# Performance work log

Hardware: AMD Instinct MI355X
Metric: run time of the kernel (lower is better)

The kernel has to match this reference:

```python
import jax, jax.numpy as jnp
import numpy as np

B, L, D = 16, 2048, 128
NEG = -1.0e9


def setup_inputs() -> dict:
    key = jax.random.key(0)
    kq, kk, kv, km = jax.random.split(key, 4)
    Q = jax.random.normal(kq, (B, L, D), dtype=jnp.float32)
    K = jax.random.normal(kk, (B, L, D), dtype=jnp.float32)
    V = jax.random.normal(kv, (B, L, D), dtype=jnp.float32)
    scale = jnp.float32(1.0 / np.sqrt(D))
    # original code masks rows where (mask + 1) == 0, i.e. mask == -1
    mask = jnp.where(jax.random.uniform(km, (B, L)) < 0.1, -1, 0).astype(jnp.int32)
    return {"Q": Q, "K": K, "V": V, "scale": scale, "mask": mask}


def reference(Q, K, V, scale, mask):
    # attention = Q @ K^T * scale  -> [B, Lq, Lk]
    att = jnp.einsum("bqd,bkd->bqk", Q, K) * scale
    # mask[b, i] broadcast over the key dim j (row-wise masking, as in the
    # original unsqueeze(-1).expand pattern with square attention)
    row_masked = (mask + 1) == 0  # [B, L]
    att = jnp.where(row_masked[:, :, None], NEG, att)
    att = jax.nn.softmax(att, axis=-1)
    context = jnp.einsum("bqk,bkd->bqd", att, V)
    return context
```

## Files before the change

kernel.cpp:

```cpp
#include <hip/hip_runtime.h>


#define NB 16
#define LL 2048
#define DD 128
#define LOG2E 1.44269504f
#define NM (-9.0f * 1.44269504f)

typedef __attribute__((ext_vector_type(8))) short short8;
typedef __attribute__((ext_vector_type(16))) float f32x16;

__device__ __forceinline__ float wexp2(float x) {
  float r; asm("v_exp_f32 %0, %1" : "=v"(r) : "v"(x)); return r;
}
__device__ __forceinline__ unsigned cvtpk(float lo, float hi) {
  unsigned r; asm("v_cvt_pk_bf16_f32 %0, %1, %2" : "=v"(r) : "v"(lo), "v"(hi)); return r;
}
__device__ __forceinline__ void gll16(const void* g, const void* l) {
  __builtin_amdgcn_global_load_lds(
      (const __attribute__((address_space(1))) unsigned*)g,
      (__attribute__((address_space(3))) unsigned*)l, 16, 0, 0);
}

__global__ void prep_kv(const float* __restrict__ K, const float* __restrict__ V,
                        short* __restrict__ Kb, short* __restrict__ Vt) {
  __shared__ short lds[64 * 130];
  int bid = blockIdx.x;
  int t = threadIdx.x;
  if (bid < 2048) {
    int g = bid * 256 + t;
    const float4* kp = (const float4*)K + (size_t)g * 2;
    float4 a = kp[0], c = kp[1];
    ((uint4*)Kb)[g] = make_uint4(cvtpk(a.x, a.y), cvtpk(a.z, a.w),
                                 cvtpk(c.x, c.y), cvtpk(c.z, c.w));
    return;
  }
  int vb = bid - 2048;
  int b = vb >> 5;
  int t0 = (vb & 31) * 64;
  #pragma unroll
  for (int i = 0; i < 8; ++i) {
    int c = t + i * 256;
    int kv = c >> 5, ds = (c & 31) * 4;
    float4 v = *(const float4*)(V + ((size_t)(b * LL + t0 + kv) * DD + ds));
    unsigned* dst = (unsigned*)(&lds[kv * 130 + ds]);
    dst[0] = cvtpk(v.x, v.y);
    dst[1] = cvtpk(v.z, v.w);
  }
  __syncthreads();
  int d = t >> 1, hf = t & 1;
  unsigned dw[16];
  #pragma unroll
  for (int i = 0; i < 16; ++i) {
    int kv = hf * 32 + i * 2;
    unsigned lo16 = (unsigned short)lds[kv * 130 + d];
    unsigned hi16 = (unsigned short)lds[(kv + 1) * 130 + d];
    dw[i] = lo16 | (hi16 << 16);
  }
  short* orow = Vt + (size_t)(b * DD + d) * LL + t0 + hf * 32;
  #pragma unroll
  for (int i = 0; i < 4; ++i)
    ((uint4*)orow)[i] = make_uint4(dw[4 * i], dw[4 * i + 1], dw[4 * i + 2], dw[4 * i + 3]);
}

__global__ __launch_bounds__(256, 2) void attn_main(
    const float* __restrict__ Q, const float* __restrict__ scl,
    const int* __restrict__ mask, const short* __restrict__ Kb,
    const short* __restrict__ Vt, float* __restrict__ Out) {
  __shared__ __align__(16) char smem[66304];
  const int tid = threadIdx.x;
  const int w = tid >> 6, l = tid & 63, lo = l & 31, hi = l >> 5;
  const int qg = w & 1, kvh = w >> 1;

  int lg = (blockIdx.x & 7) * 64 + (blockIdx.x >> 3);
  int b = lg >> 5;
  int q0 = (lg & 31) * 64 + qg * 32;

  const char* kgb = (const char*)(Kb + (size_t)b * (LL * DD));
  const char* vgb = (const char*)(Vt + (size_t)b * (LL * DD));

#define STAGE(bi_, kv0_) do { \
    char* kbuf = smem + (bi_) * 16384; \
    char* vbuf = smem + 32768 + (bi_) * 16384; \
    _Pragma("unroll") \
    for (int i = 0; i < 4; ++i) { \
      int cbk = w * 4 + i; \
      int kr = cbk * 4 + (l >> 4); \
      int kc = ((l & 15) << 4) ^ ((kr & 15) << 4); \
      gll16(kgb + (size_t)((kv0_) + kr) * 256 + kc, kbuf + cbk * 1024); \
      int vr = cbk * 8 + (l >> 3); \
      int vc = ((l & 7) << 4) ^ ((vr & 7) << 4); \
      gll16(vgb + (size_t)vr * 4096 + (size_t)(kv0_) * 2 + vc, vbuf + cbk * 1024); \
    } \
  } while (0)

  STAGE(0, 0);

  int qrow = b * LL + q0 + lo;
  float msc = (mask[qrow] == -1) ? 0.f : scl[0];
  short8 qf[8];
  {
    const float* qp = Q + (size_t)qrow * DD + hi * 8;
    #pragma unroll
    for (int dc = 0; dc < 8; ++dc) {
      float4 a = *(const float4*)(qp + dc * 16);
      float4 c = *(const float4*)(qp + dc * 16 + 4);
      union { unsigned u[4]; short8 s; } pu;
      pu.u[0] = cvtpk(a.x * msc, a.y * msc);
      pu.u[1] = cvtpk(a.z * msc, a.w * msc);
      pu.u[2] = cvtpk(c.x * msc, c.y * msc);
      pu.u[3] = cvtpk(c.z * msc, c.w * msc);
      qf[dc] = pu.s;
    }
  }

  f32x16 oacc[4];
  #pragma unroll
  for (int dt = 0; dt < 4; ++dt)
    #pragma unroll
    for (int r = 0; r < 16; ++r) oacc[dt][r] = 0.f;
  float lsum = 0.f;

  const int swzk = (lo & 15) << 4;
  const int swzv = (lo & 7) << 4;

  #pragma unroll 1
  for (int t = 0; t < 32; ++t) {
    __builtin_amdgcn_s_barrier();
    if (t < 31) {
      STAGE((t + 1) & 1, (t + 1) * 64);
      asm volatile("s_waitcnt vmcnt(8)" ::: "memory");
    } else {
      asm volatile("s_waitcnt vmcnt(0)" ::: "memory");
    }
    __builtin_amdgcn_s_barrier();
    __builtin_amdgcn_sched_barrier(0);

    const char* kb = smem + (t & 1) * 16384;
    const char* vb = smem + 32768 + (t & 1) * 16384;

    f32x16 acc;
    #pragma unroll
    for (int r = 0; r < 16; ++r) acc[r] = 0.f;
    const char* krow = kb + (kvh * 32 + lo) * 256;
    #pragma unroll
    for (int dc = 0; dc < 8; ++dc) {
      short8 kf = *(const short8*)(krow + ((dc * 32 + hi * 16) ^ swzk));
      acc = __builtin_amdgcn_mfma_f32_32x32x16_bf16(kf, qf[dc], acc, 0, 0, 0);
    }
    float ps = 0.f;
    #pragma unroll
    for (int r = 0; r < 16; ++r) {
      float p = wexp2(__builtin_fmaf(acc[r], LOG2E, NM));
      acc[r] = p; ps += p;
    }
    lsum += ps;
    short8 pa[2];
    #pragma unroll
    for (int ks = 0; ks < 2; ++ks) {
      unsigned a0 = cvtpk(acc[ks * 8 + 0], acc[ks * 8 + 1]);
      unsigned b0 = cvtpk(acc[ks * 8 + 4], acc[ks * 8 + 5]);
      unsigned c0 = cvtpk(acc[ks * 8 + 2], acc[ks * 8 + 3]);
      unsigned d0 = cvtpk(acc[ks * 8 + 6], acc[ks * 8 + 7]);
      asm volatile("v_permlane32_swap_b32 %0, %1" : "+v"(a0), "+v"(b0));
      asm volatile("v_permlane32_swap_b32 %0, %1" : "+v"(c0), "+v"(d0));
      union { unsigned u[4]; short8 s; } pu;
      pu.u[0] = a0; pu.u[1] = c0; pu.u[2] = b0; pu.u[3] = d0;
      pa[ks] = pu.s;
    }
    #pragma unroll
    for (int dt = 0; dt < 4; ++dt) {
      const char* vrow = vb + (dt * 32 + lo) * 128;
      #pragma unroll
      for (int ks = 0; ks < 2; ++ks) {
        short8 vf = *(const short8*)(vrow + ((kvh * 64 + ks * 32 + hi * 16) ^ swzv));
        oacc[dt] = __builtin_amdgcn_mfma_f32_32x32x16_bf16(pa[ks], vf, oacc[dt], 0, 0, 0);
      }
    }
  }
#undef STAGE

  float* lsb = (float*)(smem + 65536);
  float* rdb = (float*)(smem + 65536 + 512);
  __syncthreads();
  if (kvh == 1) {
    char* reg = smem + qg * 16384;
    #pragma unroll
    for (int dt = 0; dt < 4; ++dt)
      #pragma unroll
      for (int i = 0; i < 4; ++i)
        *(float4*)(reg + l * 256 + ((dt * 64 + i * 16) ^ ((l & 15) << 4))) =
            make_float4(oacc[dt][4 * i], oacc[dt][4 * i + 1],
                        oacc[dt][4 * i + 2], oacc[dt][4 * i + 3]);
    lsb[qg * 64 + l] = lsum;
  }
  __syncthreads();
  if (kvh == 0) {
    char* reg = smem + qg * 16384;
    lsum += lsb[qg * 64 + l];
    #pragma unroll
    for (int dt = 0; dt < 4; ++dt)
      #pragma unroll
      for (int i = 0; i < 4; ++i) {
        float4 p = *(const float4*)(reg + l * 256 + ((dt * 64 + i * 16) ^ ((l & 15) << 4)));
        oacc[dt][4 * i + 0] += p.x;
        oacc[dt][4 * i + 1] += p.y;
        oacc[dt][4 * i + 2] += p.z;
        oacc[dt][4 * i + 3] += p.w;
      }
    float lt = lsum + __shfl_xor(lsum, 32);
    float rd = 1.0f / lt;
    if (l < 32) rdb[qg * 32 + l] = rd;
    #pragma unroll
    for (int r = 0; r < 16; ++r) {
      int cr = (r & 3) + 8 * (r >> 2) + 4 * hi;
      float rr = rdb[qg * 32 + cr];
      float* op = Out + (size_t)(b * LL + q0 + cr) * DD + lo;
      #pragma unroll
      for (int dt = 0; dt < 4; ++dt)
        op[dt * 32] = oacc[dt][r] * rr;
    }
  }
}

extern "C" void kernel_launch(void* const* d_in, const int* in_sizes, int n_in,
                              void* d_out, int out_size, void* d_ws, size_t ws_size,
                              hipStream_t stream) {
  const float* Q = (const float*)d_in[0];
  const float* K = (const float*)d_in[1];
  const float* V = (const float*)d_in[2];
  const float* scale = (const float*)d_in[3];
  const int* mask = (const int*)d_in[4];
  float* out = (float*)d_out;

  const size_t tensor_elems = (size_t)NB * LL * DD;
  const size_t need = 2 * tensor_elems * sizeof(short);
  if (ws_size < need) return;

  short* Kbp = (short*)d_ws;
  short* Vtp = Kbp + tensor_elems;

  hipLaunchKernelGGL(prep_kv, dim3(2560), dim3(256), 0, stream, K, V, Kbp, Vtp);
  hipLaunchKernelGGL(attn_main, dim3(512), dim3(256), 0, stream, Q, scale, mask, Kbp, Vtp, out);
}
```

Before: 64.51 us.

## Restructure KV staging: contiguous LDS fill, alternate traversal direction, single barrier per tile

The STAGE macro now assigns contiguous 16-byte chunks per thread with a new V swizzle that packs two d-rows per 256-byte LDS row, and V fragment addressing is updated to match. Alternating blocks walk the KV tiles in reverse order, which spreads L2/HBM access across different tiles at the same time. The loop now waits vmcnt(0) and issues one barrier before launching the next tile's prefetch, instead of two barriers. This trades some prefetch overlap depth for fewer synchronisations and aims for better LDS write and read bank behaviour.

```diff
diff --git a/kernel.cpp b/kernel.cpp
--- a/kernel.cpp
+++ b/kernel.cpp
@@ -75,6 +75,7 @@
   int lg = (blockIdx.x & 7) * 64 + (blockIdx.x >> 3);
   int b = lg >> 5;
   int q0 = (lg & 31) * 64 + qg * 32;
+  const int rev = (blockIdx.x >> 3) & 1;
 
   const char* kgb = (const char*)(Kb + (size_t)b * (LL * DD));
   const char* vgb = (const char*)(Vt + (size_t)b * (LL * DD));
@@ -84,17 +85,19 @@
     char* vbuf = smem + 32768 + (bi_) * 16384; \
     _Pragma("unroll") \
     for (int i = 0; i < 4; ++i) { \
-      int cbk = w * 4 + i; \
-      int kr = cbk * 4 + (l >> 4); \
-      int kc = ((l & 15) << 4) ^ ((kr & 15) << 4); \
-      gll16(kgb + (size_t)((kv0_) + kr) * 256 + kc, kbuf + cbk * 1024); \
-      int vr = cbk * 8 + (l >> 3); \
-      int vc = ((l & 7) << 4) ^ ((vr & 7) << 4); \
-      gll16(vgb + (size_t)vr * 4096 + (size_t)(kv0_) * 2 + vc, vbuf + cbk * 1024); \
+      int c = tid + i * 256; \
+      int kr = c >> 4; \
+      int ks_ = c & 15; \
+      int kc = (ks_ << 4) ^ ((kr & 15) << 4); \
+      gll16(kgb + (size_t)((kv0_) + kr) * 256 + kc, kbuf + c * 16); \
+      int tt_ = ks_ ^ (kr & 15); \
+      int vd = 2 * kr + (tt_ >> 3); \
+      gll16(vgb + (size_t)vd * 4096 + (size_t)(kv0_) * 2 + (tt_ & 7) * 16, \
+            vbuf + c * 16); \
     } \
   } while (0)
 
-  STAGE(0, 0);
+  STAGE(0, (rev ? 31 : 0) * 64);
 
   int qrow = b * LL + q0 + lo;
   float msc = (mask[qrow] == -1) ? 0.f : scl[0];
@@ -122,22 +125,17 @@
   float lsum = 0.f;
 
   const int swzk = (lo & 15) << 4;
-  const int swzv = (lo & 7) << 4;
 
   #pragma unroll 1
-  for (int t = 0; t < 32; ++t) {
-    __builtin_amdgcn_s_barrier();
-    if (t < 31) {
-      STAGE((t + 1) & 1, (t + 1) * 64);
-      asm volatile("s_waitcnt vmcnt(8)" ::: "memory");
-    } else {
-      asm volatile("s_waitcnt vmcnt(0)" ::: "memory");
-    }
+  for (int u = 0; u < 32; ++u) {
+    asm volatile("s_waitcnt vmcnt(0)" ::: "memory");
     __builtin_amdgcn_s_barrier();
     __builtin_amdgcn_sched_barrier(0);
-
-    const char* kb = smem + (t & 1) * 16384;
-    const char* vb = smem + 32768 + (t & 1) * 16384;
+    int tile = rev ? (31 - u) : u;
+    if (u < 31) STAGE((u + 1) & 1, (rev ? (tile - 1) : (tile + 1)) * 64);
+
+    const char* kb = smem + (u & 1) * 16384;
+    const char* vb = smem + 32768 + (u & 1) * 16384;
 
     f32x16 acc;
     #pragma unroll
@@ -170,10 +168,11 @@
     }
     #pragma unroll
     for (int dt = 0; dt < 4; ++dt) {
-      const char* vrow = vb + (dt * 32 + lo) * 128;
+      const char* vrow = vb + (dt * 16 + (lo >> 1)) * 256;
+      const int tb = (lo & 1) * 8 + kvh * 4 + hi;
       #pragma unroll
       for (int ks = 0; ks < 2; ++ks) {
-        short8 vf = *(const short8*)(vrow + ((kvh * 64 + ks * 32 + hi * 16) ^ swzv));
+        short8 vf = *(const short8*)(vrow + (((tb + ks * 2) ^ (lo >> 1)) << 4));
         oacc[dt] = __builtin_amdgcn_mfma_f32_32x32x16_bf16(pa[ks], vf, oacc[dt], 0, 0, 0);
       }
     }
```

Result: no change. 64.06 us (-0.7%).
